# Optimization experiments

Measured on AMD Instinct MI355X. Metric: run time of the kernel, lower is better.

The kernel has to match this reference:

```python
import jax, jax.numpy as jnp
import numpy as np

PS = 16          # patch size
NFREQ = 2        # PatchExtractor Fourier frequencies -> 4 + 8*F = 20 channels
E = 8            # num experts
CAP_FACTOR = 1.25


def _pos_feats(h, w, ps, F=NFREQ, dtype=jnp.float32):
    """Fourier positional features per patch pixel: [h*w, 4+8F, ps, ps]."""
    H, W = h * ps, w * ps
    r = jnp.arange(h, dtype=dtype)
    c = jnp.arange(w, dtype=dtype)
    i = jnp.arange(ps, dtype=dtype)
    j = jnp.arange(ps, dtype=dtype)
    gy = (r[:, None, None, None] * ps + i[None, None, :, None]) / H
    gx = (c[None, :, None, None] * ps + j[None, None, None, :]) / W
    pcy = (r[:, None, None, None] + 0.5) / h
    pcx = (c[None, :, None, None] + 0.5) / w
    gy, gx, pcy, pcx = [jnp.broadcast_to(t, (h, w, ps, ps)) for t in (gy, gx, pcy, pcx)]
    feats = [gx, gy, pcx, pcy]
    for f in range(F):
        s = (2.0 ** f) * 2.0 * jnp.pi
        for t in (gx, gy, pcx, pcy):
            feats += [jnp.sin(s * t), jnp.cos(s * t)]
    out = jnp.stack(feats, 0)                       # [4+8F, h, w, ps, ps]
    return out.transpose(1, 2, 0, 3, 4).reshape(h * w, 4 + 8 * F, ps, ps)


def setup_inputs() -> dict:
    key = jax.random.key(0)
    ks = jax.random.split(key, 5)
    X = jax.random.normal(ks[0], (16, 3, 256, 256), jnp.float32)
    expert_w = jax.random.normal(ks[1], (E, 8, 3, 3, 3), jnp.float32) * 0.1   # [E, Cout, Cin, kh, kw]
    expert_b = jnp.zeros((E, 8), jnp.float32)
    gate_w = jax.random.normal(ks[2], (E, 23), jnp.float32) * 0.1             # 1x1 gate conv, mean-pooled
    gate_b = jnp.zeros((E,), jnp.float32)
    lin_w = jax.random.normal(ks[3], (512, 1000), jnp.float32) * 0.02
    lin_b = jnp.zeros((1000,), jnp.float32)
    return dict(X=X, expert_w=expert_w, expert_b=expert_b, gate_w=gate_w,
                gate_b=gate_b, lin_w=lin_w, lin_b=lin_b)


def reference(X, expert_w, expert_b, gate_w, gate_b, lin_w, lin_b):
    B, C, H, W = X.shape
    h, w = H // PS, W // PS
    P = h * w
    N = B * P
    Ccap = int(np.ceil(N * CAP_FACTOR / E))

    # 1. patch extraction: [B,C,H,W] -> [N, C, ps, ps]
    Xp = X.reshape(B, C, h, PS, w, PS).transpose(0, 2, 4, 1, 3, 5).reshape(N, C, PS, PS)

    # patch coords = patch pixels + Fourier positional channels -> [N, C+20, ps, ps]
    pos = _pos_feats(h, w, PS, dtype=X.dtype)
    coords = jnp.concatenate([Xp, jnp.tile(pos, (B, 1, 1, 1))], axis=1)

    # 2. router: 1x1 conv + global mean pool -> logits [N, E]; top-1 capacity routing
    logits = jnp.einsum('nchw,ec->ne', coords, gate_w) / (PS * PS) + gate_b
    probs = jax.nn.softmax(logits, axis=-1)
    e_idx = jnp.argmax(probs, axis=-1)                         # [N] expert choice
    one_hot = jax.nn.one_hot(e_idx, E, dtype=jnp.int32)
    c_idx = jnp.sum(jnp.cumsum(one_hot, axis=0) * one_hot, axis=-1) - 1  # rank within expert
    valid = c_idx < Ccap
    gates = jnp.take_along_axis(probs, e_idx[:, None], axis=1)[:, 0] * valid.astype(probs.dtype)

    # 3. dispatch: scatter patches into per-expert capacity buffers (slot Ccap = dump)
    slot = jnp.where(valid, c_idx, Ccap)
    buf = jnp.zeros((E, Ccap + 1, C, PS, PS), X.dtype).at[e_idx, slot].set(Xp)
    expert_in = buf[:, :Ccap]                                  # [E, Ccap, C, ps, ps]

    # 4. per-expert conv 3x3 + bias + ReLU
    def run_expert(inp, wgt, b):
        y = jax.lax.conv_general_dilated(inp, wgt, (1, 1), 'SAME')
        return jax.nn.relu(y + b[None, :, None, None])

    yout = jax.vmap(run_expert)(expert_in, expert_w, expert_b)  # [E, Ccap, Cout, ps, ps]
    Cout = yout.shape[2]

    # 5. combine: gather each patch's expert output, weighted by gate
    out_n = gates[:, None, None, None] * yout[e_idx, jnp.minimum(c_idx, Ccap - 1)]

    # reassemble patches into full image
    img = out_n.reshape(B, h, w, Cout, PS, PS).transpose(0, 3, 1, 4, 2, 5).reshape(B, Cout, H, W)

    # switch-style aux loss: E * sum_e f_e * p_e
    f_e = jnp.mean(one_hot.astype(probs.dtype) * valid[:, None].astype(probs.dtype), axis=0)
    p_e = jnp.mean(probs, axis=0)
    aux_loss = E * jnp.sum(f_e * p_e)

    # head: adaptive avg pool to 8x8, flatten, linear
    pooled = img.reshape(B, Cout, 8, H // 8, 8, W // 8).mean(axis=(3, 5))
    feat = pooled.reshape(B, -1)
    logits_cls = feat @ lin_w + lin_b
    return logits_cls, aux_loss
```

## Files before the change

### kernel.cpp

```cpp
#include <hip/hip_runtime.h>
#include <math.h>

#define CCAP 640
#define TWO_PI 6.28318530717958647692f

__global__ __launch_bounds__(256) void k_fused(const float* __restrict__ X,
        const float* __restrict__ gw, const float* __restrict__ gb,
        const float* __restrict__ ew, const float* __restrict__ eb,
        int* __restrict__ eidx, float* __restrict__ probs,
        float* __restrict__ snc)
{
    int tid = threadIdx.x;
    int wave = tid >> 6, lane = tid & 63;
    int n = blockIdx.x * 4 + wave;
    int b = n >> 8, p = n & 255, pr = p >> 4, pc = p & 15;
    int i = lane >> 2, q = lane & 3;

    float4 px[3];
    #pragma unroll
    for (int c = 0; c < 3; ++c)
        px[c] = *(const float4*)(X +
            ((size_t)(b * 3 + c) * 256 + pr * 16 + i) * 256 + pc * 16 + q * 4);

    float S0, S1, S2;
    {
        float s0 = (px[0].x + px[0].y) + (px[0].z + px[0].w);
        float s1 = (px[1].x + px[1].y) + (px[1].z + px[1].w);
        float s2 = (px[2].x + px[2].y) + (px[2].z + px[2].w);
        #pragma unroll
        for (int off = 1; off < 64; off <<= 1) {
            s0 += __shfl_xor(s0, off, 64);
            s1 += __shfl_xor(s1, off, 64);
            s2 += __shfl_xor(s2, off, 64);
        }
        S0 = s0; S1 = s1; S2 = s2;
    }

    int m = lane & 15;
    float tx = (float)(pc * 16 + m) * (1.0f / 256.0f);
    float ty = (float)(pr * 16 + m) * (1.0f / 256.0f);
    float t0 = __sinf(TWO_PI * tx),       t1 = __cosf(TWO_PI * tx);
    float t2 = __sinf(2.f * TWO_PI * tx), t3 = __cosf(2.f * TWO_PI * tx);
    float t4 = __sinf(TWO_PI * ty),       t5 = __cosf(TWO_PI * ty);
    float t6 = __sinf(2.f * TWO_PI * ty), t7 = __cosf(2.f * TWO_PI * ty);
    #pragma unroll
    for (int off = 1; off < 16; off <<= 1) {
        t0 += __shfl_xor(t0, off, 64);  t1 += __shfl_xor(t1, off, 64);
        t2 += __shfl_xor(t2, off, 64);  t3 += __shfl_xor(t3, off, 64);
        t4 += __shfl_xor(t4, off, 64);  t5 += __shfl_xor(t5, off, 64);
        t6 += __shfl_xor(t6, off, 64);  t7 += __shfl_xor(t7, off, 64);
    }

    float pcx = ((float)pc + 0.5f) * (1.0f / 16.0f);
    float pcy = ((float)pr + 0.5f) * (1.0f / 16.0f);
    float S[23];
    S[0] = S0; S[1] = S1; S[2] = S2;
    S[3] = 16.f * ((float)pc + 0.46875f);
    S[4] = 16.f * ((float)pr + 0.46875f);
    S[5] = 256.f * pcx;  S[6] = 256.f * pcy;
    S[7]  = 16.f * t0;  S[8]  = 16.f * t1;
    S[9]  = 16.f * t4;  S[10] = 16.f * t5;
    S[11] = 256.f * __sinf(TWO_PI * pcx);  S[12] = 256.f * __cosf(TWO_PI * pcx);
    S[13] = 256.f * __sinf(TWO_PI * pcy);  S[14] = 256.f * __cosf(TWO_PI * pcy);
    S[15] = 16.f * t2;  S[16] = 16.f * t3;
    S[17] = 16.f * t6;  S[18] = 16.f * t7;
    S[19] = 256.f * __sinf(2.f * TWO_PI * pcx);  S[20] = 256.f * __cosf(2.f * TWO_PI * pcx);
    S[21] = 256.f * __sinf(2.f * TWO_PI * pcy);  S[22] = 256.f * __cosf(2.f * TWO_PI * pcy);

    float lg[8];
    float mx = -1e30f;
    #pragma unroll
    for (int ee = 0; ee < 8; ++ee) {
        float a = 0.f;
        #pragma unroll
        for (int c = 0; c < 23; ++c) a += S[c] * gw[ee * 23 + c];
        lg[ee] = a * (1.0f / 256.0f) + gb[ee];
        mx = fmaxf(mx, lg[ee]);
    }
    float den = 0.f;
    float prob[8];
    #pragma unroll
    for (int ee = 0; ee < 8; ++ee) { prob[ee] = __expf(lg[ee] - mx); den += prob[ee]; }
    float inv = 1.0f / den;
    #pragma unroll
    for (int ee = 0; ee < 8; ++ee) prob[ee] *= inv;
    int am = 0; float best = lg[0];
    #pragma unroll
    for (int ee = 1; ee < 8; ++ee) if (lg[ee] > best) { best = lg[ee]; am = ee; }

    int e = __builtin_amdgcn_readfirstlane(am);
    const float* wp = ew + (size_t)e * 216;

    float acc[8][4];
    #pragma unroll
    for (int co = 0; co < 8; ++co) {
        float bv = eb[e * 8 + co];
        #pragma unroll
        for (int k = 0; k < 4; ++k) acc[co][k] = bv;
    }

    #pragma unroll
    for (int ci = 0; ci < 3; ++ci) {
        float4 v = px[ci];
        float own[6];
        own[1] = v.x; own[2] = v.y; own[3] = v.z; own[4] = v.w;
        float L = __shfl(v.w, lane - 1, 64);
        float R = __shfl(v.x, lane + 1, 64);
        own[0] = (q == 0) ? 0.f : L;
        own[5] = (q == 3) ? 0.f : R;
        float up[6], dn[6];
        #pragma unroll
        for (int c6 = 0; c6 < 6; ++c6) {
            float u = __shfl(own[c6], lane - 4, 64);
            float d = __shfl(own[c6], lane + 4, 64);
            up[c6] = (i == 0)  ? 0.f : u;
            dn[c6] = (i == 15) ? 0.f : d;
        }
        #pragma unroll
        for (int co = 0; co < 8; ++co) {
            const float* w9 = wp + co * 27 + ci * 9;
            float w0 = w9[0], w1 = w9[1], w2 = w9[2];
            float w3 = w9[3], w4 = w9[4], w5 = w9[5];
            float w6 = w9[6], w7 = w9[7], w8 = w9[8];
            #pragma unroll
            for (int k = 0; k < 4; ++k) {
                float a = acc[co][k];
                a += up[k]  * w0 + up[k + 1]  * w1 + up[k + 2]  * w2;
                a += own[k] * w3 + own[k + 1] * w4 + own[k + 2] * w5;
                a += dn[k]  * w6 + dn[k + 1]  * w7 + dn[k + 2]  * w8;
                acc[co][k] = a;
            }
        }
    }

    float sum8[8];
    #pragma unroll
    for (int co = 0; co < 8; ++co) {
        float v = fmaxf(acc[co][0], 0.f) + fmaxf(acc[co][1], 0.f)
                + fmaxf(acc[co][2], 0.f) + fmaxf(acc[co][3], 0.f);
        #pragma unroll
        for (int off = 1; off < 64; off <<= 1) v += __shfl_xor(v, off, 64);
        sum8[co] = v;
    }

    float outv = sum8[0];
    #pragma unroll
    for (int co = 1; co < 8; ++co) outv = (lane == co) ? sum8[co] : outv;
    float pv = prob[0];
    #pragma unroll
    for (int ee = 1; ee < 8; ++ee) pv = (lane == ee) ? prob[ee] : pv;
    if (lane < 8) {
        snc[(size_t)n * 8 + lane] = outv;
        probs[(size_t)n * 8 + lane] = pv;
    }
    if (lane == 0) eidx[n] = am;
}

__global__ __launch_bounds__(256) void k_route(const int* __restrict__ eidx,
        const float* __restrict__ probs, float* __restrict__ gates,
        float* __restrict__ out_aux)
{
    int t = threadIdx.x;
    int wave = t >> 6, lane = t & 63;

    unsigned long long lo = 0ull, hi = 0ull;
    int myE[16];
    #pragma unroll
    for (int k = 0; k < 16; ++k) {
        int e = eidx[t * 16 + k];
        myE[k] = e;
        int sh = 16 * (e & 3);
        if (e < 4) lo += 1ull << sh; else hi += 1ull << sh;
    }

    float lp[8] = {0.f, 0.f, 0.f, 0.f, 0.f, 0.f, 0.f, 0.f};
    #pragma unroll
    for (int k = 0; k < 16; ++k) {
        const float4* p4 = (const float4*)(probs + (size_t)(t * 16 + k) * 8);
        float4 a = p4[0], c = p4[1];
        lp[0] += a.x; lp[1] += a.y; lp[2] += a.z; lp[3] += a.w;
        lp[4] += c.x; lp[5] += c.y; lp[6] += c.z; lp[7] += c.w;
    }

    unsigned long long slo = lo, shi = hi;
    #pragma unroll
    for (int off = 1; off < 64; off <<= 1) {
        unsigned long long a = __shfl_up(slo, off, 64);
        unsigned long long c = __shfl_up(shi, off, 64);
        if (lane >= off) { slo += a; shi += c; }
    }

    __shared__ unsigned long long wlo[4], whi[4];
    __shared__ float pred[4][8];
    if (lane == 63) { wlo[wave] = slo; whi[wave] = shi; }

    #pragma unroll
    for (int ee = 0; ee < 8; ++ee) {
        float v = lp[ee];
        #pragma unroll
        for (int off = 1; off < 64; off <<= 1) v += __shfl_xor(v, off, 64);
        lp[ee] = v;
    }
    if (lane == 0) {
        pred[wave][0] = lp[0]; pred[wave][1] = lp[1];
        pred[wave][2] = lp[2]; pred[wave][3] = lp[3];
        pred[wave][4] = lp[4]; pred[wave][5] = lp[5];
        pred[wave][6] = lp[6]; pred[wave][7] = lp[7];
    }
    __syncthreads();

    unsigned long long plo = 0ull, phi = 0ull;
    #pragma unroll
    for (int w2 = 0; w2 < 4; ++w2)
        if (w2 < wave) { plo += wlo[w2]; phi += whi[w2]; }
    unsigned long long elo = plo + (slo - lo);
    unsigned long long ehi = phi + (shi - hi);

    #pragma unroll
    for (int k = 0; k < 16; ++k) {
        int nn = t * 16 + k;
        int e = myE[k];
        int sh = 16 * (e & 3);
        unsigned long long cur = (e < 4) ? elo : ehi;
        int r = (int)((cur >> sh) & 0xFFFFull);
        gates[nn] = (r < CCAP) ? probs[(size_t)nn * 8 + e] : 0.0f;
        unsigned long long inc = 1ull << sh;
        if (e < 4) elo += inc; else ehi += inc;
    }

    if (t == 0) {
        unsigned long long tl = wlo[0] + wlo[1] + wlo[2] + wlo[3];
        unsigned long long th = whi[0] + whi[1] + whi[2] + whi[3];
        float aux = 0.f;
        #pragma unroll
        for (int ee = 0; ee < 8; ++ee) {
            int tot = (ee < 4) ? (int)((tl >> (16 * ee)) & 0xFFFFull)
                               : (int)((th >> (16 * (ee - 4))) & 0xFFFFull);
            float fe = (float)min(tot, CCAP) * (1.0f / 4096.0f);
            float pe = (pred[0][ee] + pred[1][ee] + pred[2][ee] + pred[3][ee])
                       * (1.0f / 4096.0f);
            aux += fe * pe;
        }
        out_aux[0] = 8.0f * aux;
    }
}

__global__ __launch_bounds__(256) void k_cls(const float* __restrict__ snc,
        const float* __restrict__ gates, const float* __restrict__ lw,
        const float* __restrict__ lb, float* __restrict__ out)
{
    int b = blockIdx.x;
    int chunk = blockIdx.y;
    int tid = threadIdx.x;
    __shared__ float feat[512];
    __shared__ float part[128][2];

    for (int f = tid; f < 512; f += 256) {
        int co = f >> 6, rem = f & 63, py = rem >> 3, pxx = rem & 7;
        float sum = 0.f;
        #pragma unroll
        for (int dy = 0; dy < 2; ++dy)
            #pragma unroll
            for (int dx = 0; dx < 2; ++dx) {
                int nn = b * 256 + (2 * py + dy) * 16 + (2 * pxx + dx);
                sum += gates[nn] * snc[(size_t)nn * 8 + co];
            }
        feat[f] = sum * (1.0f / 1024.0f);
    }
    __syncthreads();

    int col2 = tid >> 1, half = tid & 1;
    int k = chunk * 125 + col2;
    float acc = 0.f;
    if (col2 < 125) {
        const float* lwp = lw + (size_t)(half * 256) * 1000 + k;
        const float* fp = feat + half * 256;
        #pragma unroll 8
        for (int f2 = 0; f2 < 256; ++f2) acc += fp[f2] * lwp[(size_t)f2 * 1000];
    }
    part[col2][half] = acc;
    __syncthreads();
    if (half == 0 && col2 < 125)
        out[b * 1000 + k] = part[col2][0] + part[col2][1] + lb[k];
}

extern "C" void kernel_launch(void* const* d_in, const int* in_sizes, int n_in,
                              void* d_out, int out_size, void* d_ws, size_t ws_size,
                              hipStream_t stream) {
    const float* X  = (const float*)d_in[0];
    const float* ew = (const float*)d_in[1];
    const float* eb = (const float*)d_in[2];
    const float* gw = (const float*)d_in[3];
    const float* gb = (const float*)d_in[4];
    const float* lw = (const float*)d_in[5];
    const float* lb = (const float*)d_in[6];
    float* out = (float*)d_out;

    char* ws = (char*)d_ws;
    int*   eidx  = (int*)  (ws + 0);
    float* probs = (float*)(ws + 16384);
    float* gates = (float*)(ws + 147456);
    float* snc   = (float*)(ws + 163840);

    k_fused<<<1024, 256, 0, stream>>>(X, gw, gb, ew, eb, eidx, probs, snc);
    k_route<<<1, 256, 0, stream>>>(eidx, probs, gates, out + 16000);
    k_cls<<<dim3(16, 8), 256, 0, stream>>>(snc, gates, lw, lb, out);
}
```

Measured before the change: 114.7 us.

## Fuse routing into classifier kernel and pre-reduce gate probabilities per block

Result: faster. 102.9 us (-10.3%).

```diff
diff --git a/kernel.cpp b/kernel.cpp
--- a/kernel.cpp
+++ b/kernel.cpp
@@ -7,14 +7,16 @@
 __global__ __launch_bounds__(256) void k_fused(const float* __restrict__ X,
         const float* __restrict__ gw, const float* __restrict__ gb,
         const float* __restrict__ ew, const float* __restrict__ eb,
-        int* __restrict__ eidx, float* __restrict__ probs,
-        float* __restrict__ snc)
+        int* __restrict__ eidx, float* __restrict__ ptop,
+        float* __restrict__ pspart, float* __restrict__ snc)
 {
     int tid = threadIdx.x;
     int wave = tid >> 6, lane = tid & 63;
     int n = blockIdx.x * 4 + wave;
     int b = n >> 8, p = n & 255, pr = p >> 4, pc = p & 15;
     int i = lane >> 2, q = lane & 3;
+
+    __shared__ float pb[4][8];
 
     float4 px[3];
     #pragma unroll
@@ -149,37 +151,51 @@
     float pv = prob[0];
     #pragma unroll
     for (int ee = 1; ee < 8; ++ee) pv = (lane == ee) ? prob[ee] : pv;
+    float tp = prob[0];
+    #pragma unroll
+    for (int ee = 1; ee < 8; ++ee) tp = (am == ee) ? prob[ee] : tp;
+
     if (lane < 8) {
         snc[(size_t)n * 8 + lane] = outv;
-        probs[(size_t)n * 8 + lane] = pv;
-    }
-    if (lane == 0) eidx[n] = am;
+        pb[wave][lane] = pv;
+    }
+    if (lane == 0) { eidx[n] = am; ptop[n] = tp; }
+    __syncthreads();
+    if (tid < 8)
+        pspart[(size_t)blockIdx.x * 8 + tid] =
+            pb[0][tid] + pb[1][tid] + pb[2][tid] + pb[3][tid];
 }
 
-__global__ __launch_bounds__(256) void k_route(const int* __restrict__ eidx,
-        const float* __restrict__ probs, float* __restrict__ gates,
+__global__ __launch_bounds__(256) void k_cls(const int* __restrict__ eidx,
+        const float* __restrict__ ptop, const float* __restrict__ pspart,
+        const float* __restrict__ snc, const float* __restrict__ lw,
+        const float* __restrict__ lb, float* __restrict__ out,
         float* __restrict__ out_aux)
 {
+    int b = blockIdx.x;
+    int chunk = blockIdx.y;
     int t = threadIdx.x;
     int wave = t >> 6, lane = t & 63;
 
+    __shared__ float gl[4096];
+    __shared__ float feat[512];
+    __shared__ unsigned long long wlo[4], whi[4];
+    __shared__ float part[64][4];
+    __shared__ float pred[4][8];
+
     unsigned long long lo = 0ull, hi = 0ull;
     int myE[16];
     #pragma unroll
+    for (int k4 = 0; k4 < 4; ++k4) {
+        int4 v = ((const int4*)eidx)[t * 4 + k4];
+        myE[k4 * 4 + 0] = v.x; myE[k4 * 4 + 1] = v.y;
+        myE[k4 * 4 + 2] = v.z; myE[k4 * 4 + 3] = v.w;
+    }
+    #pragma unroll
     for (int k = 0; k < 16; ++k) {
-        int e = eidx[t * 16 + k];
-        myE[k] = e;
+        int e = myE[k];
         int sh = 16 * (e & 3);
         if (e < 4) lo += 1ull << sh; else hi += 1ull << sh;
-    }
-
-    float lp[8] = {0.f, 0.f, 0.f, 0.f, 0.f, 0.f, 0.f, 0.f};
-    #pragma unroll
-    for (int k = 0; k < 16; ++k) {
-        const float4* p4 = (const float4*)(probs + (size_t)(t * 16 + k) * 8);
-        float4 a = p4[0], c = p4[1];
-        lp[0] += a.x; lp[1] += a.y; lp[2] += a.z; lp[3] += a.w;
-        lp[4] += c.x; lp[5] += c.y; lp[6] += c.z; lp[7] += c.w;
     }
 
     unsigned long long slo = lo, shi = hi;
@@ -189,24 +205,7 @@
         unsigned long long c = __shfl_up(shi, off, 64);
         if (lane >= off) { slo += a; shi += c; }
     }
-
-    __shared__ unsigned long long wlo[4], whi[4];
-    __shared__ float pred[4][8];
     if (lane == 63) { wlo[wave] = slo; whi[wave] = shi; }
-
-    #pragma unroll
-    for (int ee = 0; ee < 8; ++ee) {
-        float v = lp[ee];
-        #pragma unroll
-        for (int off = 1; off < 64; off <<= 1) v += __shfl_xor(v, off, 64);
-        lp[ee] = v;
-    }
-    if (lane == 0) {
-        pred[wave][0] = lp[0]; pred[wave][1] = lp[1];
-        pred[wave][2] = lp[2]; pred[wave][3] = lp[3];
-        pred[wave][4] = lp[4]; pred[wave][5] = lp[5];
-        pred[wave][6] = lp[6]; pred[wave][7] = lp[7];
-    }
     __syncthreads();
 
     unsigned long long plo = 0ull, phi = 0ull;
@@ -223,39 +222,13 @@
         int sh = 16 * (e & 3);
         unsigned long long cur = (e < 4) ? elo : ehi;
         int r = (int)((cur >> sh) & 0xFFFFull);
-        gates[nn] = (r < CCAP) ? probs[(size_t)nn * 8 + e] : 0.0f;
+        gl[nn] = (r < CCAP) ? ptop[nn] : 0.0f;
         unsigned long long inc = 1ull << sh;
         if (e < 4) elo += inc; else ehi += inc;
     }
-
-    if (t == 0) {
-        unsigned long long tl = wlo[0] + wlo[1] + wlo[2] + wlo[3];
-        unsigned long long th = whi[0] + whi[1] + whi[2] + whi[3];
-        float aux = 0.f;
-        #pragma unroll
-        for (int ee = 0; ee < 8; ++ee) {
-            int tot = (ee < 4) ? (int)((tl >> (16 * ee)) & 0xFFFFull)
-                               : (int)((th >> (16 * (ee - 4))) & 0xFFFFull);
-            float fe = (float)min(tot, CCAP) * (1.0f / 4096.0f);
-            float pe = (pred[0][ee] + pred[1][ee] + pred[2][ee] + pred[3][ee])
-                       * (1.0f / 4096.0f);
-            aux += fe * pe;
-        }
-        out_aux[0] = 8.0f * aux;
-    }
-}
-
-__global__ __launch_bounds__(256) void k_cls(const float* __restrict__ snc,
-        const float* __restrict__ gates, const float* __restrict__ lw,
-        const float* __restrict__ lb, float* __restrict__ out)
-{
-    int b = blockIdx.x;
-    int chunk = blockIdx.y;
-    int tid = threadIdx.x;
-    __shared__ float feat[512];
-    __shared__ float part[128][2];
-
-    for (int f = tid; f < 512; f += 256) {
+    __syncthreads();
+
+    for (int f = t; f < 512; f += 256) {
         int co = f >> 6, rem = f & 63, py = rem >> 3, pxx = rem & 7;
         float sum = 0.f;
         #pragma unroll
@@ -263,25 +236,65 @@
             #pragma unroll
             for (int dx = 0; dx < 2; ++dx) {
                 int nn = b * 256 + (2 * py + dy) * 16 + (2 * pxx + dx);
-                sum += gates[nn] * snc[(size_t)nn * 8 + co];
+                sum += gl[nn] * snc[(size_t)nn * 8 + co];
             }
         feat[f] = sum * (1.0f / 1024.0f);
     }
     __syncthreads();
 
-    int col2 = tid >> 1, half = tid & 1;
-    int k = chunk * 125 + col2;
+    int c = t & 63, quarter = t >> 6;
+    int kk = chunk * 64 + c;
+    int kcl = (kk > 999) ? 999 : kk;
     float acc = 0.f;
-    if (col2 < 125) {
-        const float* lwp = lw + (size_t)(half * 256) * 1000 + k;
-        const float* fp = feat + half * 256;
-        #pragma unroll 8
-        for (int f2 = 0; f2 < 256; ++f2) acc += fp[f2] * lwp[(size_t)f2 * 1000];
-    }
-    part[col2][half] = acc;
-    __syncthreads();
-    if (half == 0 && col2 < 125)
-        out[b * 1000 + k] = part[col2][0] + part[col2][1] + lb[k];
+    const float* lp = lw + (size_t)(quarter * 128) * 1000 + kcl;
+    const float* fp = feat + quarter * 128;
+    #pragma unroll 8
+    for (int f2 = 0; f2 < 128; ++f2) acc += fp[f2] * lp[(size_t)f2 * 1000];
+    part[c][quarter] = acc;
+    __syncthreads();
+    if (t < 64) {
+        int ko = chunk * 64 + t;
+        if (ko < 1000)
+            out[b * 1000 + ko] =
+                part[t][0] + part[t][1] + part[t][2] + part[t][3] + lb[ko];
+    }
+
+    if (b == 0 && chunk == 0) {
+        float lp8[8] = {0.f, 0.f, 0.f, 0.f, 0.f, 0.f, 0.f, 0.f};
+        for (int r = t; r < 1024; r += 256) {
+            const float4* p4 = (const float4*)(pspart + (size_t)r * 8);
+            float4 a = p4[0], d = p4[1];
+            lp8[0] += a.x; lp8[1] += a.y; lp8[2] += a.z; lp8[3] += a.w;
+            lp8[4] += d.x; lp8[5] += d.y; lp8[6] += d.z; lp8[7] += d.w;
+        }
+        #pragma unroll
+        for (int ee = 0; ee < 8; ++ee) {
+            float v = lp8[ee];
+            #pragma unroll
+            for (int off = 1; off < 64; off <<= 1) v += __shfl_xor(v, off, 64);
+            lp8[ee] = v;
+        }
+        if (lane == 0) {
+            #pragma unroll
+            for (int ee = 0; ee < 8; ++ee) pred[wave][ee] = lp8[ee];
+        }
+        __syncthreads();
+        if (t == 0) {
+            unsigned long long tl = wlo[0] + wlo[1] + wlo[2] + wlo[3];
+            unsigned long long th = whi[0] + whi[1] + whi[2] + whi[3];
+            float aux = 0.f;
+            #pragma unroll
+            for (int ee = 0; ee < 8; ++ee) {
+                int tot = (ee < 4) ? (int)((tl >> (16 * ee)) & 0xFFFFull)
+                                   : (int)((th >> (16 * (ee - 4))) & 0xFFFFull);
+                float fe = (float)min(tot, CCAP) * (1.0f / 4096.0f);
+                float pe = (pred[0][ee] + pred[1][ee] + pred[2][ee] + pred[3][ee])
+                           * (1.0f / 4096.0f);
+                aux += fe * pe;
+            }
+            out_aux[0] = 8.0f * aux;
+        }
+    }
 }
 
 extern "C" void kernel_launch(void* const* d_in, const int* in_sizes, int n_in,
@@ -297,12 +310,12 @@
     float* out = (float*)d_out;
 
     char* ws = (char*)d_ws;
-    int*   eidx  = (int*)  (ws + 0);
-    float* probs = (float*)(ws + 16384);
-    float* gates = (float*)(ws + 147456);
-    float* snc   = (float*)(ws + 163840);
-
-    k_fused<<<1024, 256, 0, stream>>>(X, gw, gb, ew, eb, eidx, probs, snc);
-    k_route<<<1, 256, 0, stream>>>(eidx, probs, gates, out + 16000);
-    k_cls<<<dim3(16, 8), 256, 0, stream>>>(snc, gates, lw, lb, out);
+    int*   eidx   = (int*)  (ws + 0);
+    float* ptop   = (float*)(ws + 16384);
+    float* pspart = (float*)(ws + 32768);
+    float* snc    = (float*)(ws + 65536);
+
+    k_fused<<<1024, 256, 0, stream>>>(X, gw, gb, ew, eb, eidx, ptop, pspart, snc);
+    k_cls<<<dim3(16, 16), 256, 0, stream>>>(eidx, ptop, pspart, snc, lw, lb,
+                                            out, out + 16000);
 }
```
